# Kernel optimization log

Measured on AMD Instinct MI355X. Metric: run time of the kernel, lower is better.

## Reference

```python
import jax, jax.numpy as jnp
import numpy as np

D = 256            # number of graph nodes (example.size(3))
K1 = D // 2        # topkpool1 k
K2 = D // 4        # topkpool2 k
B = 8


def _lrelu(x):
    return jnp.where(x > 0, x, 0.33 * x)


def _e2e(h, wa, ba, wb, bb):
    # h: [B,C,d,d]; wa,wb: [P,C,d] (squeezed (1,d)/(d,1) conv kernels)
    # cnn1: contract over columns j -> [B,P,d]; cnn2: contract over rows i -> [B,P,d]
    a = jnp.einsum('bcij,pcj->bpi', h, wa) + ba[None, :, None]
    b = jnp.einsum('bcij,pci->bpj', h, wb) + bb[None, :, None]
    # cat([a]*d, 3) + cat([b]*d, 2)  ==  broadcast-add
    return a[:, :, :, None] + b[:, :, None, :]


def _gcn(h, g, W, b):
    # h: [B,N,F_in], g: [B,N,N]; faithful to norm_g: g[i,j] / deg[j] (column-normalized
    # because torch broadcasts the [N] degree vector over the LAST dim)
    gb = (g > 0).astype(h.dtype)
    deg = gb.sum(axis=2)                      # [B,N] row sums
    gn = gb / deg[:, None, :]                 # divide column j by deg[j]
    return jnp.einsum('bij,bjf->bif', gn, h) @ W.T + b


def _pool(h, g, s, k):
    # h: [B,N,F], g: [B,N,N], s: [B,N,1] -> top-k nodes by score (descending)
    vals, idx = jax.lax.top_k(s[:, :, 0], k)              # [B,k]
    hn = jnp.take_along_axis(h, idx[:, :, None], axis=1)  # [B,k,F]
    gn = jnp.take_along_axis(g, idx[:, :, None], axis=1)
    gn = jnp.take_along_axis(gn, idx[:, None, :], axis=2) # [B,k,k]
    return hn, gn, vals[:, :, None]


def _readout(h):
    # h: [B,N,F] (node axis = 1); torch ReadOut on [B,F,N,1] max/mean over dim=2
    return jnp.concatenate([h.max(axis=1), h.mean(axis=1)], axis=1)  # [B,2F]


def _forward(x, w1a, b1a, w1b, b1b, w2a, b2a, w2b, b2b, e2n_w, e2n_b,
             a11_w, a11_b, a12_w, a12_b, g1_w, g1_b,
             a21_w, a21_b, a22_w, a22_b,
             d1_w, d1_b, d2_w, d2_b, d3_w, d3_b):
    h = _lrelu(_e2e(x, w1a, b1a, w1b, b1b))         # [B,128,d,d]
    h = _lrelu(_e2e(h, w2a, b2a, w2b, b2b))         # [B,256,d,d]
    # E2N conv (1,d): [B,8,d,1] -> node features [B,d,8]
    nodes = _lrelu(jnp.einsum('bcij,pcj->bpi', h, e2n_w) + e2n_b[None, :, None])
    nodes = jnp.transpose(nodes, (0, 2, 1))          # [B,d,8]
    g0 = x[:, 0]                                     # [B,d,d]

    w = _lrelu(_gcn(nodes, g0, a11_w, a11_b))        # [B,d,1]
    w = jax.nn.sigmoid(_gcn(w, g0, a12_w, a12_b))
    h1, g1, s1 = _pool(nodes, g0, w, K1)             # [B,K1,8], [B,K1,K1], [B,K1,1]
    out = h1 * s1 + h1
    sum1 = _readout(out)                             # [B,16]

    h2 = _gcn(out, g1, g1_w, g1_b)                   # [B,K1,8] (no activation, as in torch)
    w = _lrelu(_gcn(h2, g1, a21_w, a21_b))
    w = jax.nn.sigmoid(_gcn(w, g1, a22_w, a22_b))
    h3, g2, s2 = _pool(h2, g1, w, K2)                # [B,K2,8]
    out2 = h3 * s2 + h3
    sum2 = _readout(out2)                            # [B,16]

    z = sum1 + sum2                                  # [B,16]
    z = _lrelu(z @ d1_w.T + d1_b)                    # dropout = identity (eval mode)
    z = _lrelu(z @ d2_w.T + d2_b)
    return z @ d3_w.T + d3_b                         # [B,1]


def setup_inputs() -> dict:
    key = jax.random.key(0)
    ks = jax.random.split(key, 16)
    f32 = jnp.float32

    def rn(k, shape, scale):
        return jax.random.normal(k, shape, dtype=f32) * scale

    return {
        'x': jax.random.normal(ks[0], (B, 1, D, D), dtype=f32),
        'w1a': rn(ks[1], (128, 1, D), 0.08),  'b1a': jnp.zeros((128,), f32),
        'w1b': rn(ks[2], (128, 1, D), 0.08),  'b1b': jnp.zeros((128,), f32),
        'w2a': rn(ks[3], (256, 128, D), 0.008), 'b2a': jnp.zeros((256,), f32),
        'w2b': rn(ks[4], (256, 128, D), 0.008), 'b2b': jnp.zeros((256,), f32),
        'e2n_w': rn(ks[5], (8, 256, D), 0.005), 'e2n_b': jnp.zeros((8,), f32),
        'a11_w': rn(ks[6], (1, 8), 0.3),  'a11_b': jnp.zeros((1,), f32),
        'a12_w': rn(ks[7], (1, 1), 0.3),  'a12_b': jnp.zeros((1,), f32),
        'g1_w': rn(ks[8], (8, 8), 0.3),   'g1_b': jnp.zeros((8,), f32),
        'a21_w': rn(ks[9], (1, 8), 0.3),  'a21_b': jnp.zeros((1,), f32),
        'a22_w': rn(ks[10], (1, 1), 0.3), 'a22_b': jnp.zeros((1,), f32),
        'd1_w': rn(ks[11], (128, 16), 0.2), 'd1_b': jnp.zeros((128,), f32),
        'd2_w': rn(ks[12], (64, 128), 0.08), 'd2_b': jnp.zeros((64,), f32),
        'd3_w': rn(ks[13], (1, 64), 0.1),  'd3_b': jnp.zeros((1,), f32),
    }


def reference(x, w1a, b1a, w1b, b1b, w2a, b2a, w2b, b2b, e2n_w, e2n_b,
              a11_w, a11_b, a12_w, a12_b, g1_w, g1_b,
              a21_w, a21_b, a22_w, a22_b,
              d1_w, d1_b, d2_w, d2_b, d3_w, d3_b):
    return _forward(x, w1a, b1a, w1b, b1b, w2a, b2a, w2b, b2b, e2n_w, e2n_b,
                    a11_w, a11_b, a12_w, a12_b, g1_w, g1_b,
                    a21_w, a21_b, a22_w, a22_b,
                    d1_w, d1_b, d2_w, d2_b, d3_w, d3_b)
```

## Files before the change

### kernel.cpp

```cpp
#include <hip/hip_runtime.h>
#include <hip/hip_bf16.h>

typedef short s16x8 __attribute__((ext_vector_type(8)));
typedef float f32x4 __attribute__((ext_vector_type(4)));
typedef float f32x2 __attribute__((ext_vector_type(2)));

#define TID threadIdx.x
#define N_IN 27

__device__ __forceinline__ float bf2f(unsigned short u) {
    unsigned v = ((unsigned)u) << 16;
    return __builtin_bit_cast(float, v);
}
__device__ __forceinline__ unsigned short f2bf(float f) {
    unsigned u = __builtin_bit_cast(unsigned, f);
    u += 0x7fffu + ((u >> 16) & 1u);
    return (unsigned short)(u >> 16);
}
__device__ __forceinline__ float lrelu_f(float x) { return fmaxf(x, 0.33f * x); }

__device__ __forceinline__ unsigned hb_pair(float a, float b) {
#if __has_builtin(__builtin_amdgcn_cvt_pk_bf16_f32)
    auto pk = __builtin_amdgcn_cvt_pk_bf16_f32(a, b);
    unsigned u; __builtin_memcpy(&u, &pk, 4); return u;
#else
    return (unsigned)f2bf(a) | ((unsigned)f2bf(b) << 16);
#endif
}
__device__ __forceinline__ unsigned lrelu_pack(float pv, float qx, float qy) {
    f32x2 s; s.x = pv + qx; s.y = pv + qy;
    f32x2 m = s * 0.33f;
    f32x2 r = __builtin_elementwise_max(s, m);
    return hb_pair(r.x, r.y);
}

union FragU { s16x8 v; uint4 q; unsigned w[4]; };

__global__ __launch_bounds__(256) void k_detect(const unsigned* __restrict__ w, int* __restrict__ flag) {
    __shared__ int cnt;
    if (TID == 0) cnt = 0;
    __syncthreads();
    int c = 0;
    for (int k = TID; k < 1024; k += 256) {
        unsigned e = (w[k] >> 23) & 0xFFu;
        c += (e >= 160u) ? 1 : 0;
    }
    atomicAdd(&cnt, c);
    __syncthreads();
    if (TID == 0) *flag = (cnt > 512) ? 1 : 0;
}

struct ConvArgs {
    const void* src[N_IN];
    unsigned short* dst[N_IN];
    int n[N_IN];
};

__global__ __launch_bounds__(256) void k_convert(ConvArgs A, const int* __restrict__ flag) {
    const int t = blockIdx.y;
    const int n = A.n[t];
    const int fl = *flag;
    if (fl && n >= 1000000) return;
    unsigned short* d = A.dst[t];
    const int npair = n >> 1;
    const int stride = gridDim.x * 256;
    if (fl) {
        const unsigned* s = (const unsigned*)A.src[t];
        for (int i = blockIdx.x * 256 + TID; i < npair; i += stride) ((unsigned*)d)[i] = s[i];
        if ((n & 1) && blockIdx.x == 0 && TID == 0) d[n - 1] = ((const unsigned short*)A.src[t])[n - 1];
    } else {
        const float* s = (const float*)A.src[t];
        for (int i = blockIdx.x * 256 + TID; i < npair; i += stride) {
            unsigned u = (unsigned)f2bf(s[2 * i]) | ((unsigned)f2bf(s[2 * i + 1]) << 16);
            ((unsigned*)d)[i] = u;
        }
        if ((n & 1) && blockIdx.x == 0 && TID == 0) d[n - 1] = f2bf(s[n - 1]);
    }
}

__global__ __launch_bounds__(128) void k_l1(
    const unsigned short* __restrict__ x,
    const unsigned short* __restrict__ w1a, const unsigned short* __restrict__ b1a,
    const unsigned short* __restrict__ w1b, const unsigned short* __restrict__ b1b,
    float* __restrict__ A1, float* __restrict__ B1)
{
    const int r = blockIdx.x, b = blockIdx.y, v = blockIdx.z;
    const int tid = TID;
    __shared__ float xr[256];
    const unsigned short* xb = x + b * 65536;
    if (v == 0) {
        xr[tid]       = bf2f(xb[r * 256 + tid]);
        xr[tid + 128] = bf2f(xb[r * 256 + tid + 128]);
    } else {
        xr[tid]       = bf2f(xb[tid * 256 + r]);
        xr[tid + 128] = bf2f(xb[(tid + 128) * 256 + r]);
    }
    __syncthreads();
    const unsigned short* w    = v ? w1b : w1a;
    const unsigned short* bias = v ? b1b : b1a;
    float* OUT = v ? B1 : A1;
    float acc = bf2f(bias[tid]);
    const unsigned short* wr = w + tid * 256;
    #pragma unroll 4
    for (int q = 0; q < 256; q += 8) {
        uint4 pk = *(const uint4*)(wr + q);
        unsigned ww0 = pk.x, ww1 = pk.y, ww2 = pk.z, ww3 = pk.w;
        acc += xr[q + 0] * bf2f((unsigned short)ww0) + xr[q + 1] * bf2f((unsigned short)(ww0 >> 16));
        acc += xr[q + 2] * bf2f((unsigned short)ww1) + xr[q + 3] * bf2f((unsigned short)(ww1 >> 16));
        acc += xr[q + 4] * bf2f((unsigned short)ww2) + xr[q + 5] * bf2f((unsigned short)(ww2 >> 16));
        acc += xr[q + 6] * bf2f((unsigned short)ww3) + xr[q + 7] * bf2f((unsigned short)(ww3 >> 16));
    }
    OUT[b * 32768 + tid * 256 + r] = acc;
}

__global__ __launch_bounds__(256) void k_e2e(
    const float* __restrict__ A1, const float* __restrict__ B1,
    const unsigned short* __restrict__ w2a_m, const unsigned short* __restrict__ w2b_m,
    const unsigned short* __restrict__ w2a_r, const unsigned short* __restrict__ w2b_r,
    const int* __restrict__ flag,
    float* __restrict__ part)
{
    const int rt = blockIdx.x;
    const int s  = blockIdx.y;
    const int bw = blockIdx.z;
    const int b = bw >> 1, which = bw & 1;
    const int fl = *flag;
    const float* P = (which ? B1 : A1) + b * 32768;
    const float* Q = (which ? A1 : B1) + b * 32768;
    const unsigned short* W = which ? (fl ? w2b_r : w2b_m) : (fl ? w2a_r : w2a_m);
    const int c0 = s * 16, r0 = rt * 128;

    __shared__ float Qs[16][256];
    __shared__ float Ps[16][128];

    const int tid = TID;
    {
        const float4* Qg = (const float4*)(Q + c0 * 256);
        float4* Qd = (float4*)&Qs[0][0];
        #pragma unroll
        for (int k = 0; k < 4; ++k) Qd[tid + k * 256] = Qg[tid + k * 256];
        #pragma unroll
        for (int k = 0; k < 2; ++k) {
            int i = tid + k * 256;
            int row = i >> 5, col = i & 31;
            *(float4*)&Ps[row][col * 4] = *(const float4*)&P[(c0 + row) * 256 + r0 + col * 4];
        }
    }
    __syncthreads();

    const int wave = tid >> 6, lane = tid & 63, quad = lane >> 4, l16 = lane & 15;
    const int pbase = wave * 64;

    f32x4 acc[4][8] = {};

    for (int c = 0; c < 16; ++c) {
        float pv[8];
        #pragma unroll
        for (int nf = 0; nf < 8; ++nf) pv[nf] = Ps[c][nf * 16 + l16];
        const unsigned short* Wc = W + (size_t)(c0 + c) * 256;
        #pragma unroll
        for (int q0 = 0; q0 < 8; ++q0) {
            float4 qa = *(const float4*)&Qs[c][q0 * 32 + quad * 8];
            float4 qb = *(const float4*)&Qs[c][q0 * 32 + quad * 8 + 4];
            FragU af[4];
            #pragma unroll
            for (int pf = 0; pf < 4; ++pf)
                af[pf].q = *(const uint4*)(Wc + (size_t)(pbase + pf * 16 + l16) * 32768 + q0 * 32 + quad * 8);
            #pragma unroll
            for (int nf = 0; nf < 8; ++nf) {
                FragU hb;
                hb.w[0] = lrelu_pack(pv[nf], qa.x, qa.y);
                hb.w[1] = lrelu_pack(pv[nf], qa.z, qa.w);
                hb.w[2] = lrelu_pack(pv[nf], qb.x, qb.y);
                hb.w[3] = lrelu_pack(pv[nf], qb.z, qb.w);
                #pragma unroll
                for (int pf = 0; pf < 4; ++pf)
                    acc[pf][nf] = __builtin_amdgcn_mfma_f32_16x16x32_bf16(af[pf].v, hb.v, acc[pf][nf], 0, 0, 0);
            }
        }
    }
    float* pb = part + (size_t)(s * 16 + bw) * 65536;
    #pragma unroll
    for (int pf = 0; pf < 4; ++pf)
        #pragma unroll
        for (int nf = 0; nf < 8; ++nf)
            #pragma unroll
            for (int t = 0; t < 4; ++t) {
                int p = pbase + pf * 16 + quad * 4 + t;
                int r = r0 + nf * 16 + l16;
                pb[p * 256 + r] = acc[pf][nf][t];
            }
}

__global__ __launch_bounds__(256) void k_red(
    const float* __restrict__ part,
    const unsigned short* __restrict__ b2a, const unsigned short* __restrict__ b2b,
    float* __restrict__ A2, float* __restrict__ B2)
{
    const int bw = blockIdx.y; const int b = bw >> 1, which = bw & 1;
    const int idx = blockIdx.x * 256 + TID;
    const float4* pp = (const float4*)part;
    float4 acc = make_float4(0.f, 0.f, 0.f, 0.f);
    #pragma unroll
    for (int s = 0; s < 8; ++s) {
        float4 v = pp[(size_t)(s * 16 + bw) * 16384 + idx];
        acc.x += v.x; acc.y += v.y; acc.z += v.z; acc.w += v.w;
    }
    const int p = idx >> 6;
    const float bias = bf2f((which ? b2b : b2a)[p]);
    acc.x += bias; acc.y += bias; acc.z += bias; acc.w += bias;
    float* OUT = (which ? B2 : A2) + b * 65536;
    ((float4*)OUT)[idx] = acc;
}

__global__ __launch_bounds__(256) void k_e2n(
    const float* __restrict__ A2, const float* __restrict__ B2,
    const unsigned short* __restrict__ e2nw,
    float* __restrict__ nodes_raw)
{
    const int it = blockIdx.x, b = blockIdx.y, sn = blockIdx.z;
    const int tid = TID, wave = tid >> 6, lane = tid & 63, quad = lane >> 4, l16 = lane & 15;
    const int i0 = it * 16;
    const int c0 = sn * 32 + wave * 8;
    const float* Ab = A2 + b * 65536;
    const float* Bb = B2 + b * 65536;
    f32x4 acc = {};
    for (int cc = 0; cc < 8; ++cc) {
        const int c = c0 + cc;
        const float pv = Ab[c * 256 + i0 + l16];
        const float* Brow = Bb + c * 256;
        const unsigned short* Wrow = e2nw + (size_t)l16 * 65536 + c * 256;
        #pragma unroll
        for (int q0 = 0; q0 < 8; ++q0) {
            float4 qa = *(const float4*)&Brow[q0 * 32 + quad * 8];
            float4 qb = *(const float4*)&Brow[q0 * 32 + quad * 8 + 4];
            FragU a;
            if (l16 < 8) a.q = *(const uint4*)(Wrow + q0 * 32 + quad * 8);
            else         a.q = make_uint4(0u, 0u, 0u, 0u);
            FragU hb;
            hb.w[0] = lrelu_pack(pv, qa.x, qa.y);
            hb.w[1] = lrelu_pack(pv, qa.z, qa.w);
            hb.w[2] = lrelu_pack(pv, qb.x, qb.y);
            hb.w[3] = lrelu_pack(pv, qb.z, qb.w);
            acc = __builtin_amdgcn_mfma_f32_16x16x32_bf16(a.v, hb.v, acc, 0, 0, 0);
        }
    }
    __shared__ float red[4][16][16];
    #pragma unroll
    for (int t = 0; t < 4; ++t) red[wave][quad * 4 + t][l16] = acc[t];
    __syncthreads();
    const int row = tid >> 4, col = tid & 15;
    if (row < 8) {
        float ssum = red[0][row][col] + red[1][row][col] + red[2][row][col] + red[3][row][col];
        atomicAdd(&nodes_raw[b * 2048 + (i0 + col) * 8 + row], ssum);
    }
}

__global__ __launch_bounds__(256) void k_adj(
    const unsigned short* __restrict__ xm,
    unsigned long long* __restrict__ adjw, float* __restrict__ rdegw)
{
    const int b = blockIdx.y;
    const int tid = TID, wave = tid >> 6, lane = tid & 63;
    const int rbase = blockIdx.x * 32 + wave * 8;
    for (int rr = 0; rr < 8; ++rr) {
        const int row = rbase + rr;
        int d = 0;
        unsigned long long w[4];
        #pragma unroll
        for (int k = 0; k < 4; ++k) {
            float v = bf2f(xm[b * 65536 + row * 256 + k * 64 + lane]);
            w[k] = __ballot(v > 0.0f);
            d += __popcll(w[k]);
        }
        if (lane == 0) {
            #pragma unroll
            for (int k = 0; k < 4; ++k) adjw[(b * 256 + row) * 4 + k] = w[k];
            rdegw[b * 256 + row] = d ? 1.0f / (float)d : 0.0f;
        }
    }
}

__global__ __launch_bounds__(256) void k_tail(
    const unsigned long long* __restrict__ adjw, const float* __restrict__ rdegw,
    const float* __restrict__ nodes_raw, const unsigned short* __restrict__ e2n_b,
    const unsigned short* __restrict__ a11_w, const unsigned short* __restrict__ a11_b,
    const unsigned short* __restrict__ a12_w, const unsigned short* __restrict__ a12_b,
    const unsigned short* __restrict__ g1_w,  const unsigned short* __restrict__ g1_b,
    const unsigned short* __restrict__ a21_w, const unsigned short* __restrict__ a21_b,
    const unsigned short* __restrict__ a22_w, const unsigned short* __restrict__ a22_b,
    const unsigned short* __restrict__ d1_w,  const unsigned short* __restrict__ d1_b,
    const unsigned short* __restrict__ d2_w,  const unsigned short* __restrict__ d2_b,
    const unsigned short* __restrict__ d3_w,  const unsigned short* __restrict__ d3_b,
    const int* __restrict__ flag,
    void* __restrict__ outv)
{
    const int b = blockIdx.x;
    const int tid = TID;

    __shared__ unsigned long long adj[256][4];
    __shared__ float nod[256][8];
    __shared__ float rdeg[256];
    __shared__ float md[256];
    __shared__ float w1s[256];
    __shared__ float w2s[256];
    __shared__ int   selflag[256];
    __shared__ int   selidx[128];
    __shared__ float s1v[128];
    __shared__ float out1[128][8];
    __shared__ float aggL[128][8];
    __shared__ float h2L[128][8];
    __shared__ unsigned long long adj1[128][2];
    __shared__ float rdeg1[128];
    __shared__ float tA[128];
    __shared__ float w1t[128];
    __shared__ float w2t[128];
    __shared__ int   sel2flag[128];
    __shared__ int   sel2idx[64];
    __shared__ float s2v[64];
    __shared__ float out2[64][8];
    __shared__ float r1[16], r2[16], zz[16];
    __shared__ float z1[128];
    __shared__ float z2[64];

    if (tid < 128) { selidx[tid] = 0; s1v[tid] = 0.0f; }
    if (tid < 64)  { sel2idx[tid] = 0; s2v[tid] = 0.0f; }

    {
        #pragma unroll
        for (int k = 0; k < 4; ++k) adj[tid][k] = adjw[(b * 256 + tid) * 4 + k];
        rdeg[tid] = rdegw[b * 256 + tid];
        for (int f = 0; f < 8; ++f)
            nod[tid][f] = lrelu_f(nodes_raw[b * 2048 + tid * 8 + f] + bf2f(e2n_b[f]));
    }
    __syncthreads();
    {
        float s = 0.0f;
        for (int f = 0; f < 8; ++f) s += nod[tid][f] * bf2f(a11_w[f]);
        md[tid] = s * rdeg[tid];
    }
    __syncthreads();
    {
        float s = 0.0f;
        for (int k = 0; k < 4; ++k) {
            unsigned long long m = adj[tid][k];
            while (m) { int j = __builtin_ctzll(m); m &= m - 1; s += md[k * 64 + j]; }
        }
        w1s[tid] = lrelu_f(s + bf2f(a11_b[0]));
    }
    __syncthreads();
    md[tid] = w1s[tid] * bf2f(a12_w[0]) * rdeg[tid];
    __syncthreads();
    {
        float s = 0.0f;
        for (int k = 0; k < 4; ++k) {
            unsigned long long m = adj[tid][k];
            while (m) { int j = __builtin_ctzll(m); m &= m - 1; s += md[k * 64 + j]; }
        }
        w2s[tid] = 1.0f / (1.0f + expf(-(s + bf2f(a12_b[0]))));
    }
    __syncthreads();
    {
        const float my = w2s[tid];
        int cnt = 0;
        for (int j = 0; j < 256; ++j) {
            float o = w2s[j];
            cnt += (o > my) || (o == my && j < tid);
        }
        selflag[tid] = (cnt < 128) ? 1 : 0;
    }
    __syncthreads();
    if (selflag[tid]) {
        int pos = 0;
        for (int j = 0; j < tid; ++j) pos += selflag[j];
        if (pos < 128) { selidx[pos] = tid; s1v[pos] = w2s[tid]; }
    }
    __syncthreads();
    for (int k = tid; k < 1024; k += 256) {
        int t = k >> 3, f = k & 7;
        out1[t][f] = nod[selidx[t]][f] * (1.0f + s1v[t]);
    }
    __syncthreads();
    if (tid < 16) {
        int f = tid & 7;
        if (tid < 8) {
            float mx = -INFINITY;
            for (int t = 0; t < 128; ++t) mx = fmaxf(mx, out1[t][f]);
            r1[tid] = mx;
        } else {
            float s = 0.0f;
            for (int t = 0; t < 128; ++t) s += out1[t][f];
            r1[tid] = s * (1.0f / 128.0f);
        }
    }
    if (tid < 128) {
        unsigned long long wds[2] = {0ull, 0ull};
        const int gi = selidx[tid];
        for (int u = 0; u < 128; ++u) {
            const int gj = selidx[u];
            unsigned long long bit = (adj[gi][gj >> 6] >> (gj & 63)) & 1ull;
            wds[u >> 6] |= bit << (u & 63);
        }
        adj1[tid][0] = wds[0]; adj1[tid][1] = wds[1];
        int d = __popcll(wds[0]) + __popcll(wds[1]);
        rdeg1[tid] = d ? 1.0f / (float)d : 0.0f;
    }
    __syncthreads();
    {
        const int t = tid >> 1, f0 = (tid & 1) * 4;
        float a0 = 0, a1 = 0, a2 = 0, a3 = 0;
        for (int k = 0; k < 2; ++k) {
            unsigned long long m = adj1[t][k];
            while (m) {
                int u = __builtin_ctzll(m); m &= m - 1;
                int uu = k * 64 + u;
                float rr = rdeg1[uu];
                a0 += out1[uu][f0 + 0] * rr;
                a1 += out1[uu][f0 + 1] * rr;
                a2 += out1[uu][f0 + 2] * rr;
                a3 += out1[uu][f0 + 3] * rr;
            }
        }
        aggL[t][f0 + 0] = a0; aggL[t][f0 + 1] = a1; aggL[t][f0 + 2] = a2; aggL[t][f0 + 3] = a3;
    }
    __syncthreads();
    for (int k = tid; k < 1024; k += 256) {
        int t = k >> 3, fo = k & 7;
        float s = bf2f(g1_b[fo]);
        for (int f = 0; f < 8; ++f) s += aggL[t][f] * bf2f(g1_w[fo * 8 + f]);
        h2L[t][fo] = s;
    }
    __syncthreads();
    if (tid < 128) {
        float s = 0.0f;
        for (int f = 0; f < 8; ++f) s += h2L[tid][f] * bf2f(a21_w[f]);
        tA[tid] = s * rdeg1[tid];
    }
    __syncthreads();
    if (tid < 128) {
        float s = 0.0f;
        for (int k = 0; k < 2; ++k) {
            unsigned long long m = adj1[tid][k];
            while (m) { int u = __builtin_ctzll(m); m &= m - 1; s += tA[k * 64 + u]; }
        }
        w1t[tid] = lrelu_f(s + bf2f(a21_b[0]));
    }
    __syncthreads();
    if (tid < 128) tA[tid] = w1t[tid] * bf2f(a22_w[0]) * rdeg1[tid];
    __syncthreads();
    if (tid < 128) {
        float s = 0.0f;
        for (int k = 0; k < 2; ++k) {
            unsigned long long m = adj1[tid][k];
            while (m) { int u = __builtin_ctzll(m); m &= m - 1; s += tA[k * 64 + u]; }
        }
        w2t[tid] = 1.0f / (1.0f + expf(-(s + bf2f(a22_b[0]))));
    }
    __syncthreads();
    if (tid < 128) {
        const float my = w2t[tid];
        int cnt = 0;
        for (int u = 0; u < 128; ++u) {
            float o = w2t[u];
            cnt += (o > my) || (o == my && u < tid);
        }
        sel2flag[tid] = (cnt < 64) ? 1 : 0;
    }
    __syncthreads();
    if (tid < 128 && sel2flag[tid]) {
        int pos = 0;
        for (int u = 0; u < tid; ++u) pos += sel2flag[u];
        if (pos < 64) { sel2idx[pos] = tid; s2v[pos] = w2t[tid]; }
    }
    __syncthreads();
    for (int k = tid; k < 512; k += 256) {
        int u = k >> 3, f = k & 7;
        out2[u][f] = h2L[sel2idx[u]][f] * (1.0f + s2v[u]);
    }
    __syncthreads();
    if (tid < 16) {
        int f = tid & 7;
        if (tid < 8) {
            float mx = -INFINITY;
            for (int t = 0; t < 64; ++t) mx = fmaxf(mx, out2[t][f]);
            r2[tid] = mx;
        } else {
            float s = 0.0f;
            for (int t = 0; t < 64; ++t) s += out2[t][f];
            r2[tid] = s * (1.0f / 64.0f);
        }
    }
    __syncthreads();
    if (tid < 16) zz[tid] = r1[tid] + r2[tid];
    __syncthreads();
    if (tid < 128) {
        float s = bf2f(d1_b[tid]);
        for (int k = 0; k < 16; ++k) s += zz[k] * bf2f(d1_w[tid * 16 + k]);
        z1[tid] = lrelu_f(s);
    }
    __syncthreads();
    if (tid < 64) {
        float s = bf2f(d2_b[tid]);
        for (int k = 0; k < 128; ++k) s += z1[k] * bf2f(d2_w[tid * 128 + k]);
        z2[tid] = lrelu_f(s);
    }
    __syncthreads();
    if (tid == 0) {
        float s = bf2f(d3_b[0]);
        for (int k = 0; k < 64; ++k) s += z2[k] * bf2f(d3_w[k]);
        if (*flag) ((unsigned short*)outv)[b] = f2bf(s);
        else       ((float*)outv)[b] = s;
    }
}

extern "C" void kernel_launch(void* const* d_in, const int* in_sizes, int n_in,
                              void* d_out, int out_size, void* d_ws, size_t ws_size,
                              hipStream_t stream) {
    float* ws        = (float*)d_ws;
    float* A1        = ws;
    float* B1        = ws + 262144;
    float* A2        = ws + 524288;
    float* B2        = ws + 1048576;
    float* nodes_raw = ws + 1572864;
    float* rdegw     = ws + 1589248;
    int*   flag      = (int*)(ws + 1597440);
    unsigned long long* adjw = (unsigned long long*)(ws + 1597444);
    float* part      = ws + 1613832;
    unsigned short* mbase = (unsigned short*)(ws + 10002440);

    unsigned short* mir[N_IN];
    ConvArgs CA;
    {
        size_t off = 0;
        for (int i = 0; i < N_IN; ++i) {
            off = (off + 7) & ~(size_t)7;
            mir[i] = mbase + off;
            off += (size_t)in_sizes[i];
            CA.src[i] = d_in[i];
            CA.dst[i] = mir[i];
            CA.n[i]   = in_sizes[i];
        }
    }

    k_detect<<<dim3(1), 256, 0, stream>>>((const unsigned*)d_in[5], flag);
    k_convert<<<dim3(256, N_IN), 256, 0, stream>>>(CA, flag);
    hipMemsetAsync(nodes_raw, 0, 16384 * sizeof(float), stream);
    k_l1<<<dim3(256, 8, 2), 128, 0, stream>>>(mir[0], mir[1], mir[2], mir[3], mir[4], A1, B1);
    k_adj<<<dim3(8, 8), 256, 0, stream>>>(mir[0], adjw, rdegw);
    k_e2e<<<dim3(2, 8, 16), 256, 0, stream>>>(A1, B1,
        mir[5], mir[7],
        (const unsigned short*)d_in[5], (const unsigned short*)d_in[7],
        flag, part);
    k_red<<<dim3(64, 16), 256, 0, stream>>>(part, mir[6], mir[8], A2, B2);
    k_e2n<<<dim3(16, 8, 8), 256, 0, stream>>>(A2, B2, mir[9], nodes_raw);
    k_tail<<<dim3(8), 256, 0, stream>>>(adjw, rdegw, nodes_raw, mir[10],
        mir[11], mir[12], mir[13], mir[14], mir[15], mir[16], mir[17], mir[18],
        mir[19], mir[20], mir[21], mir[22], mir[23], mir[24], mir[25], mir[26],
        flag, d_out);
}
```

Measured before the change: 441.4 us.

## Split e2e block across 8 waves and use inline bf16 pack conversion

k_e2e now launches 512 threads and arranges its 8 waves as a 4x2 grid over output channels and rows. Each wave holds a 4x4 accumulator tile instead of 4x8, which halves register pressure and should raise occupancy and latency hiding. The bf16 packing now always uses an inline v_cvt_pk_bf16_f32 instruction, including in the convert kernel, and the shared-memory Q reads use f32x2 loads. In exchange, every W fragment is loaded by two waves instead of one, which adds redundant global/L2 traffic.

After: 446.6 us. No clear change (+1.2%).

```diff
diff --git a/kernel.cpp b/kernel.cpp
--- a/kernel.cpp
+++ b/kernel.cpp
@@ -19,19 +19,13 @@
 }
 __device__ __forceinline__ float lrelu_f(float x) { return fmaxf(x, 0.33f * x); }
 
-__device__ __forceinline__ unsigned hb_pair(float a, float b) {
-#if __has_builtin(__builtin_amdgcn_cvt_pk_bf16_f32)
-    auto pk = __builtin_amdgcn_cvt_pk_bf16_f32(a, b);
-    unsigned u; __builtin_memcpy(&u, &pk, 4); return u;
-#else
-    return (unsigned)f2bf(a) | ((unsigned)f2bf(b) << 16);
-#endif
-}
-__device__ __forceinline__ unsigned lrelu_pack(float pv, float qx, float qy) {
-    f32x2 s; s.x = pv + qx; s.y = pv + qy;
+__device__ __forceinline__ unsigned lrelu_pack(float pv, f32x2 q) {
+    f32x2 s = q + pv;
     f32x2 m = s * 0.33f;
     f32x2 r = __builtin_elementwise_max(s, m);
-    return hb_pair(r.x, r.y);
+    unsigned u;
+    asm("v_cvt_pk_bf16_f32 %0, %1, %2" : "=v"(u) : "v"(r.x), "v"(r.y));
+    return u;
 }
 
 union FragU { s16x8 v; uint4 q; unsigned w[4]; };
@@ -71,7 +65,9 @@
     } else {
         const float* s = (const float*)A.src[t];
         for (int i = blockIdx.x * 256 + TID; i < npair; i += stride) {
-            unsigned u = (unsigned)f2bf(s[2 * i]) | ((unsigned)f2bf(s[2 * i + 1]) << 16);
+            unsigned u;
+            float a = s[2 * i], b = s[2 * i + 1];
+            asm("v_cvt_pk_bf16_f32 %0, %1, %2" : "=v"(u) : "v"(a), "v"(b));
             ((unsigned*)d)[i] = u;
         }
         if ((n & 1) && blockIdx.x == 0 && TID == 0) d[n - 1] = f2bf(s[n - 1]);
@@ -113,7 +109,7 @@
     OUT[b * 32768 + tid * 256 + r] = acc;
 }
 
-__global__ __launch_bounds__(256) void k_e2e(
+__global__ __launch_bounds__(512) void k_e2e(
     const float* __restrict__ A1, const float* __restrict__ B1,
     const unsigned short* __restrict__ w2a_m, const unsigned short* __restrict__ w2b_m,
     const unsigned short* __restrict__ w2a_r, const unsigned short* __restrict__ w2b_r,
@@ -137,42 +133,43 @@
     {
         const float4* Qg = (const float4*)(Q + c0 * 256);
         float4* Qd = (float4*)&Qs[0][0];
+        Qd[tid]       = Qg[tid];
+        Qd[tid + 512] = Qg[tid + 512];
+        int row = tid >> 5, col = tid & 31;
+        *(float4*)&Ps[row][col * 4] = *(const float4*)&P[(c0 + row) * 256 + r0 + col * 4];
+    }
+    __syncthreads();
+
+    const int wave = tid >> 6, lane = tid & 63, quad = lane >> 4, l16 = lane & 15;
+    const int wi = wave & 3, wj = wave >> 2;
+    const int pbase = wi * 64;
+    const int rbase = wj * 64;
+
+    f32x4 acc[4][4] = {};
+
+    const unsigned short* Wrow[4];
+    #pragma unroll
+    for (int pf = 0; pf < 4; ++pf)
+        Wrow[pf] = W + (size_t)(pbase + pf * 16 + l16) * 32768 + c0 * 256;
+
+    for (int c = 0; c < 16; ++c) {
+        float pv[4];
         #pragma unroll
-        for (int k = 0; k < 4; ++k) Qd[tid + k * 256] = Qg[tid + k * 256];
-        #pragma unroll
-        for (int k = 0; k < 2; ++k) {
-            int i = tid + k * 256;
-            int row = i >> 5, col = i & 31;
-            *(float4*)&Ps[row][col * 4] = *(const float4*)&P[(c0 + row) * 256 + r0 + col * 4];
-        }
-    }
-    __syncthreads();
-
-    const int wave = tid >> 6, lane = tid & 63, quad = lane >> 4, l16 = lane & 15;
-    const int pbase = wave * 64;
-
-    f32x4 acc[4][8] = {};
-
-    for (int c = 0; c < 16; ++c) {
-        float pv[8];
-        #pragma unroll
-        for (int nf = 0; nf < 8; ++nf) pv[nf] = Ps[c][nf * 16 + l16];
-        const unsigned short* Wc = W + (size_t)(c0 + c) * 256;
+        for (int nf = 0; nf < 4; ++nf) pv[nf] = Ps[c][rbase + nf * 16 + l16];
         #pragma unroll
         for (int q0 = 0; q0 < 8; ++q0) {
-            float4 qa = *(const float4*)&Qs[c][q0 * 32 + quad * 8];
-            float4 qb = *(const float4*)&Qs[c][q0 * 32 + quad * 8 + 4];
+            const f32x2* qp = (const f32x2*)&Qs[c][q0 * 32 + quad * 8];
             FragU af[4];
             #pragma unroll
             for (int pf = 0; pf < 4; ++pf)
-                af[pf].q = *(const uint4*)(Wc + (size_t)(pbase + pf * 16 + l16) * 32768 + q0 * 32 + quad * 8);
+                af[pf].q = *(const uint4*)(Wrow[pf] + c * 256 + q0 * 32 + quad * 8);
             #pragma unroll
-            for (int nf = 0; nf < 8; ++nf) {
+            for (int nf = 0; nf < 4; ++nf) {
                 FragU hb;
-                hb.w[0] = lrelu_pack(pv[nf], qa.x, qa.y);
-                hb.w[1] = lrelu_pack(pv[nf], qa.z, qa.w);
-                hb.w[2] = lrelu_pack(pv[nf], qb.x, qb.y);
-                hb.w[3] = lrelu_pack(pv[nf], qb.z, qb.w);
+                hb.w[0] = lrelu_pack(pv[nf], qp[0]);
+                hb.w[1] = lrelu_pack(pv[nf], qp[1]);
+                hb.w[2] = lrelu_pack(pv[nf], qp[2]);
+                hb.w[3] = lrelu_pack(pv[nf], qp[3]);
                 #pragma unroll
                 for (int pf = 0; pf < 4; ++pf)
                     acc[pf][nf] = __builtin_amdgcn_mfma_f32_16x16x32_bf16(af[pf].v, hb.v, acc[pf][nf], 0, 0, 0);
@@ -183,11 +180,11 @@
     #pragma unroll
     for (int pf = 0; pf < 4; ++pf)
         #pragma unroll
-        for (int nf = 0; nf < 8; ++nf)
+        for (int nf = 0; nf < 4; ++nf)
             #pragma unroll
             for (int t = 0; t < 4; ++t) {
                 int p = pbase + pf * 16 + quad * 4 + t;
-                int r = r0 + nf * 16 + l16;
+                int r = r0 + rbase + nf * 16 + l16;
                 pb[p * 256 + r] = acc[pf][nf][t];
             }
 }
@@ -232,16 +229,15 @@
         const unsigned short* Wrow = e2nw + (size_t)l16 * 65536 + c * 256;
         #pragma unroll
         for (int q0 = 0; q0 < 8; ++q0) {
-            float4 qa = *(const float4*)&Brow[q0 * 32 + quad * 8];
-            float4 qb = *(const float4*)&Brow[q0 * 32 + quad * 8 + 4];
+            const f32x2* qp = (const f32x2*)&Brow[q0 * 32 + quad * 8];
             FragU a;
             if (l16 < 8) a.q = *(const uint4*)(Wrow + q0 * 32 + quad * 8);
             else         a.q = make_uint4(0u, 0u, 0u, 0u);
             FragU hb;
-            hb.w[0] = lrelu_pack(pv, qa.x, qa.y);
-            hb.w[1] = lrelu_pack(pv, qa.z, qa.w);
-            hb.w[2] = lrelu_pack(pv, qb.x, qb.y);
-            hb.w[3] = lrelu_pack(pv, qb.z, qb.w);
+            hb.w[0] = lrelu_pack(pv, qp[0]);
+            hb.w[1] = lrelu_pack(pv, qp[1]);
+            hb.w[2] = lrelu_pack(pv, qp[2]);
+            hb.w[3] = lrelu_pack(pv, qp[3]);
             acc = __builtin_amdgcn_mfma_f32_16x16x32_bf16(a.v, hb.v, acc, 0, 0, 0);
         }
     }
@@ -547,7 +543,7 @@
     hipMemsetAsync(nodes_raw, 0, 16384 * sizeof(float), stream);
     k_l1<<<dim3(256, 8, 2), 128, 0, stream>>>(mir[0], mir[1], mir[2], mir[3], mir[4], A1, B1);
     k_adj<<<dim3(8, 8), 256, 0, stream>>>(mir[0], adjw, rdegw);
-    k_e2e<<<dim3(2, 8, 16), 256, 0, stream>>>(A1, B1,
+    k_e2e<<<dim3(2, 8, 16), 512, 0, stream>>>(A1, B1,
         mir[5], mir[7],
         (const unsigned short*)d_in[5], (const unsigned short*)d_in[7],
         flag, part);
```
